# Kernel optimization log

Hardware: AMD Instinct MI355X
Metric: run time of the kernel (lower is better)

The kernel has to match this reference:

```python
import jax, jax.numpy as jnp
import numpy as np
import math

INPUT_SIZE = 64  # feature dim D, matches init_kwargs input_size


def setup_inputs() -> dict:
    key = jax.random.key(0)
    k1, k2 = jax.random.split(key)
    B, N, D = 32, 2048, INPUT_SIZE
    x = jax.random.normal(k1, (B, N, D), dtype=jnp.float32)
    adj = jax.random.randint(k2, (N, N), 0, 2, dtype=jnp.int32)
    return {"input": x, "adj": adj}


def reference(input, adj):
    # input: [B, N, D], adj: [N, N]
    scale = 1.0 / math.sqrt(INPUT_SIZE)
    # batched QK^T: [B, N, N]
    scores = jnp.einsum('bnd,bmd->bnm', input, input) * scale
    neg = jnp.float32(-1e12)
    masked = jnp.where(adj > 0, scores, neg)  # adj broadcasts over batch
    attn = jax.nn.softmax(masked, axis=-1)
    # AV: [B, N, D]
    out = jnp.einsum('bnm,bmd->bnd', attn, input)
    return out
```

## Files before the change

### kernel.cpp

```cpp
#include <hip/hip_runtime.h>
#include <hip/hip_bf16.h>

#define NB 32
#define NN 2048
#define DD 64
#define NCH 32
#define LOG2E 1.44269504088896340736f

typedef __attribute__((ext_vector_type(8))) short short8;
typedef __attribute__((ext_vector_type(4))) short short4v;
typedef __attribute__((ext_vector_type(4))) float f32x4;

#define MFMA32K(A, B, C) \
  __builtin_amdgcn_mfma_f32_16x16x32_bf16((A), (B), (C), 0, 0, 0)
#define MFMA16(A, B, C) \
  __builtin_amdgcn_mfma_f32_16x16x16bf16_1k((A), (B), (C), 0, 0, 0)

#define GLOAD_LDS16(gp, lp)                                                   \
  __builtin_amdgcn_global_load_lds(                                          \
      (const __attribute__((address_space(1))) void*)(gp),                   \
      (__attribute__((address_space(3))) void*)(lp), 16, 0, 0)

__device__ __forceinline__ short f2bf(float x) {
  __bf16 h = (__bf16)x;
  return __builtin_bit_cast(short, h);
}

__device__ __forceinline__ float fast_exp2(float x) {
#if __has_builtin(__builtin_amdgcn_exp2f)
  return __builtin_amdgcn_exp2f(x);
#else
  return exp2f(x);
#endif
}

__global__ __launch_bounds__(256) void prep_img(const float* __restrict__ x,
                                                short* __restrict__ img) {
  __shared__ short t[64 * 72];
  const int tid = threadIdx.x;
  const int c = blockIdx.x;
  const int b = blockIdx.y;
  const int r = tid >> 2;
  const int cg = tid & 3;

  const float* src = x + ((size_t)b * NN + c * 64 + r) * DD + cg * 16;
#pragma unroll
  for (int h = 0; h < 2; ++h) {
    float4 f0 = ((const float4*)src)[h * 2];
    float4 f1 = ((const float4*)src)[h * 2 + 1];
    short8 a;
    a[0] = f2bf(f0.x); a[1] = f2bf(f0.y); a[2] = f2bf(f0.z); a[3] = f2bf(f0.w);
    a[4] = f2bf(f1.x); a[5] = f2bf(f1.y); a[6] = f2bf(f1.z); a[7] = f2bf(f1.w);
    *(short8*)&t[r * 72 + cg * 16 + h * 8] = a;
  }
  __syncthreads();

  short* imgc = img + (size_t)(b * NCH + c) * 16 * 512;

#pragma unroll
  for (int i = 0; i < 2; ++i) {
    const int kc = tid + i * 256;
    const int u = kc >> 6, l = kc & 63;
    const int nt = u >> 1, ks = u & 1;
    short8 v = *(const short8*)&t[(nt * 16 + (l & 15)) * 72 + ks * 32 +
                                  (l >> 4) * 8];
    *(short8*)&imgc[(size_t)u * 512 + l * 8] = v;
  }
#pragma unroll
  for (int i = 0; i < 2; ++i) {
    const int vc = tid + i * 256;
    const int u = vc >> 6, l = vc & 63;
    const int dt = u >> 1, ntp = u & 1;
    const int d = dt * 16 + (l & 15);
    const int k0 = ntp * 32 + ((l >> 4) << 2);
    short8 o;
#pragma unroll
    for (int h = 0; h < 2; ++h)
#pragma unroll
      for (int r2 = 0; r2 < 4; ++r2)
        o[h * 4 + r2] = t[(k0 + h * 16 + r2) * 72 + d];
    *(short8*)&imgc[(size_t)(8 + u) * 512 + l * 8] = o;
  }
}

__global__ __launch_bounds__(256) void prep_adj(const int* __restrict__ adj,
                                                unsigned long long* __restrict__ bits) {
  const int i = blockIdx.x * 256 + threadIdx.x;
  unsigned long long m = __ballot(adj[i] > 0);
  if ((threadIdx.x & 63) == 0) bits[i >> 6] = m;
}

__global__ __launch_bounds__(256, 2) void gat_flash6(
    const float* __restrict__ x, const short* __restrict__ img,
    const unsigned long long* __restrict__ adjb, float* __restrict__ out) {
  __shared__ short sI[2][8192];

  const int tid = threadIdx.x;
  const int w = tid >> 6;
  const int l = tid & 63;
  const int lane16 = l & 15;
  const int quad = l >> 4;
  const int b = blockIdx.y;
  const int qbase = blockIdx.x * 128 + w * 32;

  const float qs = 0.125f * LOG2E;
  short8 qf[2][2];
#pragma unroll
  for (int qt = 0; qt < 2; ++qt) {
    const float* qp = x + ((size_t)b * NN + qbase + qt * 16 + lane16) * DD;
#pragma unroll
    for (int ks = 0; ks < 2; ++ks) {
      float4 v0 = *(const float4*)(qp + ks * 32 + quad * 8);
      float4 v1 = *(const float4*)(qp + ks * 32 + quad * 8 + 4);
      short8 a;
      a[0] = f2bf(v0.x * qs); a[1] = f2bf(v0.y * qs);
      a[2] = f2bf(v0.z * qs); a[3] = f2bf(v0.w * qs);
      a[4] = f2bf(v1.x * qs); a[5] = f2bf(v1.y * qs);
      a[6] = f2bf(v1.z * qs); a[7] = f2bf(v1.w * qs);
      qf[qt][ks] = a;
    }
  }

  f32x4 acc[2][4];
  f32x4 acc_l[2];
#pragma unroll
  for (int qt = 0; qt < 2; ++qt) {
    acc_l[qt] = {0.f, 0.f, 0.f, 0.f};
#pragma unroll
    for (int dt = 0; dt < 4; ++dt) acc[qt][dt] = {0.f, 0.f, 0.f, 0.f};
  }
  short4v ones;
  ones[0] = 0x3F80; ones[1] = 0x3F80; ones[2] = 0x3F80; ones[3] = 0x3F80;

  const short* img_b = img + (size_t)b * NCH * 16 * 512;
  const unsigned long long* ar0 = adjb + (size_t)(qbase + lane16) * NCH;
  const unsigned long long* ar1 = adjb + (size_t)(qbase + 16 + lane16) * NCH;

#pragma unroll
  for (int i = 0; i < 4; ++i) {
    const int u = i * 4 + w;
    GLOAD_LDS16(img_b + (size_t)u * 512 + l * 8, &sI[0][u * 512]);
  }
  __syncthreads();

  for (int c = 0; c < NCH; ++c) {
    const int cur = c & 1;
    if (c + 1 < NCH) {
#pragma unroll
      for (int i = 0; i < 4; ++i) {
        const int u = i * 4 + w;
        GLOAD_LDS16(img_b + ((size_t)(c + 1) * 16 + u) * 512 + l * 8,
                    &sI[cur ^ 1][u * 512]);
      }
    }

    const unsigned long long a0 = ar0[c] >> (quad * 4);
    const unsigned long long a1 = ar1[c] >> (quad * 4);
    const unsigned lo0 = (unsigned)a0, hi0 = (unsigned)(a0 >> 32);
    const unsigned lo1 = (unsigned)a1, hi1 = (unsigned)(a1 >> 32);

    const short* sK = sI[cur];
    const short* sV = sI[cur] + 4096;

#pragma unroll
    for (int ntp = 0; ntp < 2; ++ntp) {
      short4v pf[2][2];
#pragma unroll
      for (int h = 0; h < 2; ++h) {
        const int nt = ntp * 2 + h;
        f32x4 s0 = {0.f, 0.f, 0.f, 0.f};
        f32x4 s1 = {0.f, 0.f, 0.f, 0.f};
#pragma unroll
        for (int ks = 0; ks < 2; ++ks) {
          short8 kf = *(const short8*)&sK[(nt * 2 + ks) * 512 + l * 8];
          s0 = MFMA32K(kf, qf[0][ks], s0);
          s1 = MFMA32K(kf, qf[1][ks], s1);
        }
        const unsigned w0 = (nt < 2) ? lo0 : hi0;
        const unsigned w1 = (nt < 2) ? lo1 : hi1;
        const int sh = (nt & 1) * 16;
#pragma unroll
        for (int r = 0; r < 4; ++r) {
          float e0 = fast_exp2(s0[r]);
          float e1 = fast_exp2(s1[r]);
          float p0 = ((w0 >> (sh + r)) & 1u) ? e0 : 0.f;
          float p1 = ((w1 >> (sh + r)) & 1u) ? e1 : 0.f;
          pf[h][0][r] = f2bf(p0);
          pf[h][1][r] = f2bf(p1);
        }
        acc_l[0] = MFMA16(ones, pf[h][0], acc_l[0]);
        acc_l[1] = MFMA16(ones, pf[h][1], acc_l[1]);
      }
#pragma unroll
      for (int dt = 0; dt < 4; ++dt) {
        short8 vv = *(const short8*)&sV[(dt * 2 + ntp) * 512 + l * 8];
        short4v vlo, vhi;
        vlo[0] = vv[0]; vlo[1] = vv[1]; vlo[2] = vv[2]; vlo[3] = vv[3];
        vhi[0] = vv[4]; vhi[1] = vv[5]; vhi[2] = vv[6]; vhi[3] = vv[7];
        acc[0][dt] = MFMA16(vlo, pf[0][0], acc[0][dt]);
        acc[1][dt] = MFMA16(vlo, pf[0][1], acc[1][dt]);
        acc[0][dt] = MFMA16(vhi, pf[1][0], acc[0][dt]);
        acc[1][dt] = MFMA16(vhi, pf[1][1], acc[1][dt]);
      }
    }
    __syncthreads();
  }

#pragma unroll
  for (int qt = 0; qt < 2; ++qt) {
    const float inv = 1.0f / acc_l[qt][0];
    float* op =
        out + ((size_t)b * NN + qbase + qt * 16 + lane16) * DD + quad * 4;
#pragma unroll
    for (int dt = 0; dt < 4; ++dt) {
      float4 o;
      o.x = acc[qt][dt][0] * inv;
      o.y = acc[qt][dt][1] * inv;
      o.z = acc[qt][dt][2] * inv;
      o.w = acc[qt][dt][3] * inv;
      *(float4*)(op + dt * 16) = o;
    }
  }
}

extern "C" void kernel_launch(void* const* d_in, const int* in_sizes, int n_in,
                              void* d_out, int out_size, void* d_ws,
                              size_t ws_size, hipStream_t stream) {
  const float* x = (const float*)d_in[0];
  const int* adj = (const int*)d_in[1];
  float* out = (float*)d_out;

  short* img = (short*)d_ws;
  unsigned long long* adjb =
      (unsigned long long*)(img + (size_t)NB * NCH * 16 * 512);

  prep_img<<<dim3(NCH, NB), 256, 0, stream>>>(x, img);
  prep_adj<<<(NN * NN) / 256, 256, 0, stream>>>(adj, adjb);
  gat_flash6<<<dim3(NN / 128, NB), 256, 0, stream>>>(x, img, adjb, out);
}
```

Measured before the change: 149.0 us.

## Process two independent key chunks per iteration with separate accumulators

The main attention loop now runs 16 iterations, each handling two key chunks (c and c+16) into separate accumulator sets. LDS buffers grow to four, so both streams are double-buffered, and the accumulators are summed at the end. This exposes more independent MFMA and exp work per barrier and halves the number of __syncthreads. In exchange it doubles accumulator register use and LDS footprint, which may cut occupancy below the two-blocks-per-CU bound.

New measurement: 147.4 us. About the same (-1.1%).

```diff
diff --git a/kernel.cpp b/kernel.cpp
--- a/kernel.cpp
+++ b/kernel.cpp
@@ -90,10 +90,64 @@
   if ((threadIdx.x & 63) == 0) bits[i >> 6] = m;
 }
 
-__global__ __launch_bounds__(256, 2) void gat_flash6(
+__device__ __forceinline__ void chunk_body(
+    const short* __restrict__ sB, unsigned long long a0, unsigned long long a1,
+    int quad, int l, const short8 (&qf)[2][2], const short4v& ones,
+    f32x4 (&acc)[2][4], f32x4 (&acc_l)[2]) {
+  a0 >>= (quad * 4);
+  a1 >>= (quad * 4);
+  const unsigned lo0 = (unsigned)a0, hi0 = (unsigned)(a0 >> 32);
+  const unsigned lo1 = (unsigned)a1, hi1 = (unsigned)(a1 >> 32);
+  const short* sK = sB;
+  const short* sV = sB + 4096;
+
+#pragma unroll
+  for (int ntp = 0; ntp < 2; ++ntp) {
+    short4v pf[2][2];
+#pragma unroll
+    for (int h = 0; h < 2; ++h) {
+      const int nt = ntp * 2 + h;
+      f32x4 s0 = {0.f, 0.f, 0.f, 0.f};
+      f32x4 s1 = {0.f, 0.f, 0.f, 0.f};
+#pragma unroll
+      for (int ks = 0; ks < 2; ++ks) {
+        short8 kf = *(const short8*)&sK[(nt * 2 + ks) * 512 + l * 8];
+        s0 = MFMA32K(kf, qf[0][ks], s0);
+        s1 = MFMA32K(kf, qf[1][ks], s1);
+      }
+      const unsigned w0 = (nt < 2) ? lo0 : hi0;
+      const unsigned w1 = (nt < 2) ? lo1 : hi1;
+      const int sh = (nt & 1) * 16;
+#pragma unroll
+      for (int r = 0; r < 4; ++r) {
+        float e0 = fast_exp2(s0[r]);
+        float e1 = fast_exp2(s1[r]);
+        float p0 = ((w0 >> (sh + r)) & 1u) ? e0 : 0.f;
+        float p1 = ((w1 >> (sh + r)) & 1u) ? e1 : 0.f;
+        pf[h][0][r] = f2bf(p0);
+        pf[h][1][r] = f2bf(p1);
+      }
+      acc_l[0] = MFMA16(ones, pf[h][0], acc_l[0]);
+      acc_l[1] = MFMA16(ones, pf[h][1], acc_l[1]);
+    }
+#pragma unroll
+    for (int dt = 0; dt < 4; ++dt) {
+      short8 vv = *(const short8*)&sV[(dt * 2 + ntp) * 512 + l * 8];
+      short4v vlo, vhi;
+      vlo[0] = vv[0]; vlo[1] = vv[1]; vlo[2] = vv[2]; vlo[3] = vv[3];
+      vhi[0] = vv[4]; vhi[1] = vv[5]; vhi[2] = vv[6]; vhi[3] = vv[7];
+      acc[0][dt] = MFMA16(vlo, pf[0][0], acc[0][dt]);
+      acc[1][dt] = MFMA16(vlo, pf[0][1], acc[1][dt]);
+      acc[0][dt] = MFMA16(vhi, pf[1][0], acc[0][dt]);
+      acc[1][dt] = MFMA16(vhi, pf[1][1], acc[1][dt]);
+    }
+  }
+}
+
+__global__ __launch_bounds__(256, 2) void gat_flash7(
     const float* __restrict__ x, const short* __restrict__ img,
     const unsigned long long* __restrict__ adjb, float* __restrict__ out) {
-  __shared__ short sI[2][8192];
+  __shared__ short sI[4][8192];
 
   const int tid = threadIdx.x;
   const int w = tid >> 6;
@@ -121,13 +175,16 @@
     }
   }
 
-  f32x4 acc[2][4];
-  f32x4 acc_l[2];
+  f32x4 accA[2][4], accB[2][4], aclA[2], aclB[2];
 #pragma unroll
   for (int qt = 0; qt < 2; ++qt) {
-    acc_l[qt] = {0.f, 0.f, 0.f, 0.f};
-#pragma unroll
-    for (int dt = 0; dt < 4; ++dt) acc[qt][dt] = {0.f, 0.f, 0.f, 0.f};
+    aclA[qt] = {0.f, 0.f, 0.f, 0.f};
+    aclB[qt] = {0.f, 0.f, 0.f, 0.f};
+#pragma unroll
+    for (int dt = 0; dt < 4; ++dt) {
+      accA[qt][dt] = {0.f, 0.f, 0.f, 0.f};
+      accB[qt][dt] = {0.f, 0.f, 0.f, 0.f};
+    }
   }
   short4v ones;
   ones[0] = 0x3F80; ones[1] = 0x3F80; ones[2] = 0x3F80; ones[3] = 0x3F80;
@@ -140,84 +197,44 @@
   for (int i = 0; i < 4; ++i) {
     const int u = i * 4 + w;
     GLOAD_LDS16(img_b + (size_t)u * 512 + l * 8, &sI[0][u * 512]);
+    GLOAD_LDS16(img_b + (size_t)16 * 8192 + u * 512 + l * 8, &sI[2][u * 512]);
   }
   __syncthreads();
 
-  for (int c = 0; c < NCH; ++c) {
+  for (int c = 0; c < 16; ++c) {
     const int cur = c & 1;
-    if (c + 1 < NCH) {
+    if (c < 15) {
+      const short* pA = img_b + (size_t)(c + 1) * 8192;
+      const short* pB = img_b + (size_t)(c + 17) * 8192;
 #pragma unroll
       for (int i = 0; i < 4; ++i) {
         const int u = i * 4 + w;
-        GLOAD_LDS16(img_b + ((size_t)(c + 1) * 16 + u) * 512 + l * 8,
-                    &sI[cur ^ 1][u * 512]);
+        GLOAD_LDS16(pA + (size_t)u * 512 + l * 8, &sI[cur ^ 1][u * 512]);
+        GLOAD_LDS16(pB + (size_t)u * 512 + l * 8, &sI[2 + (cur ^ 1)][u * 512]);
       }
     }
 
-    const unsigned long long a0 = ar0[c] >> (quad * 4);
-    const unsigned long long a1 = ar1[c] >> (quad * 4);
-    const unsigned lo0 = (unsigned)a0, hi0 = (unsigned)(a0 >> 32);
-    const unsigned lo1 = (unsigned)a1, hi1 = (unsigned)(a1 >> 32);
-
-    const short* sK = sI[cur];
-    const short* sV = sI[cur] + 4096;
-
-#pragma unroll
-    for (int ntp = 0; ntp < 2; ++ntp) {
-      short4v pf[2][2];
-#pragma unroll
-      for (int h = 0; h < 2; ++h) {
-        const int nt = ntp * 2 + h;
-        f32x4 s0 = {0.f, 0.f, 0.f, 0.f};
-        f32x4 s1 = {0.f, 0.f, 0.f, 0.f};
-#pragma unroll
-        for (int ks = 0; ks < 2; ++ks) {
-          short8 kf = *(const short8*)&sK[(nt * 2 + ks) * 512 + l * 8];
-          s0 = MFMA32K(kf, qf[0][ks], s0);
-          s1 = MFMA32K(kf, qf[1][ks], s1);
-        }
-        const unsigned w0 = (nt < 2) ? lo0 : hi0;
-        const unsigned w1 = (nt < 2) ? lo1 : hi1;
-        const int sh = (nt & 1) * 16;
-#pragma unroll
-        for (int r = 0; r < 4; ++r) {
-          float e0 = fast_exp2(s0[r]);
-          float e1 = fast_exp2(s1[r]);
-          float p0 = ((w0 >> (sh + r)) & 1u) ? e0 : 0.f;
-          float p1 = ((w1 >> (sh + r)) & 1u) ? e1 : 0.f;
-          pf[h][0][r] = f2bf(p0);
-          pf[h][1][r] = f2bf(p1);
-        }
-        acc_l[0] = MFMA16(ones, pf[h][0], acc_l[0]);
-        acc_l[1] = MFMA16(ones, pf[h][1], acc_l[1]);
-      }
-#pragma unroll
-      for (int dt = 0; dt < 4; ++dt) {
-        short8 vv = *(const short8*)&sV[(dt * 2 + ntp) * 512 + l * 8];
-        short4v vlo, vhi;
-        vlo[0] = vv[0]; vlo[1] = vv[1]; vlo[2] = vv[2]; vlo[3] = vv[3];
-        vhi[0] = vv[4]; vhi[1] = vv[5]; vhi[2] = vv[6]; vhi[3] = vv[7];
-        acc[0][dt] = MFMA16(vlo, pf[0][0], acc[0][dt]);
-        acc[1][dt] = MFMA16(vlo, pf[0][1], acc[1][dt]);
-        acc[0][dt] = MFMA16(vhi, pf[1][0], acc[0][dt]);
-        acc[1][dt] = MFMA16(vhi, pf[1][1], acc[1][dt]);
-      }
-    }
+    const unsigned long long a0A = ar0[c], a1A = ar1[c];
+    const unsigned long long a0B = ar0[c + 16], a1B = ar1[c + 16];
+
+    chunk_body(sI[cur], a0A, a1A, quad, l, qf, ones, accA, aclA);
+    chunk_body(sI[2 + cur], a0B, a1B, quad, l, qf, ones, accB, aclB);
+
     __syncthreads();
   }
 
 #pragma unroll
   for (int qt = 0; qt < 2; ++qt) {
-    const float inv = 1.0f / acc_l[qt][0];
+    const float inv = 1.0f / (aclA[qt][0] + aclB[qt][0]);
     float* op =
         out + ((size_t)b * NN + qbase + qt * 16 + lane16) * DD + quad * 4;
 #pragma unroll
     for (int dt = 0; dt < 4; ++dt) {
       float4 o;
-      o.x = acc[qt][dt][0] * inv;
-      o.y = acc[qt][dt][1] * inv;
-      o.z = acc[qt][dt][2] * inv;
-      o.w = acc[qt][dt][3] * inv;
+      o.x = (accA[qt][dt][0] + accB[qt][dt][0]) * inv;
+      o.y = (accA[qt][dt][1] + accB[qt][dt][1]) * inv;
+      o.z = (accA[qt][dt][2] + accB[qt][dt][2]) * inv;
+      o.w = (accA[qt][dt][3] + accB[qt][dt][3]) * inv;
       *(float4*)(op + dt * 16) = o;
     }
   }
@@ -236,5 +253,5 @@
 
   prep_img<<<dim3(NCH, NB), 256, 0, stream>>>(x, img);
   prep_adj<<<(NN * NN) / 256, 256, 0, stream>>>(adj, adjb);
-  gat_flash6<<<dim3(NN / 128, NB), 256, 0, stream>>>(x, img, adjb, out);
-}
+  gat_flash7<<<dim3(NN / 128, NB), 256, 0, stream>>>(x, img, adjb, out);
+}
```
